# Performance work log

Measured on AMD Instinct MI355X. Metric: run time of the kernel, lower is better.

The kernel has to match this reference:

```python
import jax, jax.numpy as jnp
import numpy as np


def setup_inputs() -> dict:
    key = jax.random.key(0)
    ks = jax.random.split(key, 9)
    n, L, H, H2 = 1024, 256, 512, 256
    return {
        "lstms0": jax.random.normal(ks[0], (n, L), jnp.float32),
        "lstms1": jax.random.normal(ks[1], (n, L), jnp.float32),
        "W_foh": jax.random.normal(ks[2], (2 * L, H), jnp.float32) * 0.05,
        "W_fom": jax.random.normal(ks[3], (2 * L, H), jnp.float32) * 0.05,
        "catBias": jax.random.normal(ks[4], (1, 2 * H), jnp.float32) * 0.05,
        "hid2Layer": jax.random.normal(ks[5], (2 * H, H2), jnp.float32) * 0.05,
        "hid2Bias": jax.random.normal(ks[6], (1, H2), jnp.float32) * 0.05,
        "outLayer": jax.random.normal(ks[7], (H2, 1), jnp.float32) * 0.05,
        "outBias": jax.random.normal(ks[8], (1, 1), jnp.float32) * 0.05,
    }


def reference(lstms0, lstms1, W_foh, W_fom, catBias, hid2Layer, hid2Bias, outLayer, outBias):
    act = jnp.tanh
    H = W_foh.shape[1]
    # per-token concatenated BiLSTM state: [n, 2L]
    x = jnp.concatenate([lstms0, lstms1], axis=-1)
    headfov = x @ W_foh  # [n, H]
    modfov = x @ W_fom   # [n, H]
    # activation(concat(head_i, mod_j) + catBias) is elementwise, so it splits:
    ah = act(headfov + catBias[0, :H])  # [n, H]
    am = act(modfov + catBias[0, H:])   # [n, H]
    # concat(ah_i, am_j) @ hid2Layer == ah_i @ W_top + am_j @ W_bot
    A = ah @ hid2Layer[:H]  # [n, H2]
    B = am @ hid2Layer[H:]  # [n, H2]
    # pairwise hidden: [n_head, n_mod, H2]
    Z = act(A[:, None, :] + B[None, :, :] + hid2Bias[0])
    scores = jnp.einsum("ijh,h->ij", Z, outLayer[:, 0]) + outBias[0, 0]
    return scores  # [n, n], scores[i, j] = score(head=i, mod=j)
```

## Files before the change

### kernel.cpp

```cpp
#include <hip/hip_runtime.h>
#include <hip/hip_bf16.h>

typedef short s16x4 __attribute__((ext_vector_type(4)));
typedef short s16x8 __attribute__((ext_vector_type(8)));
typedef float f32x4 __attribute__((ext_vector_type(4)));

#define LOG2E_2 2.8853900817779268f

__device__ __forceinline__ float fexp2(float x){ return __builtin_amdgcn_exp2f(x); }
__device__ __forceinline__ float frcp (float x){ return __builtin_amdgcn_rcpf(x); }
__device__ __forceinline__ float ftanh(float v){
    return 1.0f - 2.0f * frcp(1.0f + fexp2(LOG2E_2 * v));
}
__device__ __forceinline__ unsigned short f2bf(float v){
    __hip_bfloat16 h = __float2bfloat16(v);
    return __builtin_bit_cast(unsigned short, h);
}
__device__ __forceinline__ float bf2f(unsigned short u){
    return __bfloat162float(__builtin_bit_cast(__hip_bfloat16, u));
}
__device__ __forceinline__ f32x4 mfma32(s16x8 a, s16x8 b, f32x4 c){
    return __builtin_amdgcn_mfma_f32_16x16x32_bf16(a, b, c, 0, 0, 0);
}

__global__ __launch_bounds__(256) void prep_x(
    const float* __restrict__ l0, const float* __restrict__ l1,
    unsigned short* __restrict__ xhi, unsigned short* __restrict__ xlo)
{
    int idx = (blockIdx.x * 256 + threadIdx.x) * 4;
    int r = idx >> 9, c = idx & 511;
    float4 v = (c < 256) ? *(const float4*)(l0 + r*256 + c)
                         : *(const float4*)(l1 + r*256 + (c - 256));
    ushort4 h, l;
    h.x = f2bf(v.x); l.x = f2bf(v.x - bf2f(h.x));
    h.y = f2bf(v.y); l.y = f2bf(v.y - bf2f(h.y));
    h.z = f2bf(v.z); l.z = f2bf(v.z - bf2f(h.z));
    h.w = f2bf(v.w); l.w = f2bf(v.w - bf2f(h.w));
    *(ushort4*)(xhi + idx) = h;
    *(ushort4*)(xlo + idx) = l;
}

__global__ __launch_bounds__(256) void prep_wt(
    const float* __restrict__ srcA, const float* __restrict__ srcB,
    int splitN, int lda, int K,
    unsigned short* __restrict__ dhi, unsigned short* __restrict__ dlo)
{
    __shared__ float F[32][33];
    const int t = threadIdx.x;
    const int k0 = blockIdx.x * 32, n0 = blockIdx.y * 32;
    {
        int kk = t >> 3, n4 = (t & 7) * 4;
        int n = n0 + n4;
        const float* s = (n < splitN) ? (srcA + (k0+kk)*lda + n)
                                      : (srcB + (k0+kk)*lda + (n - splitN));
        float4 v = *(const float4*)s;
        F[kk][n4+0] = v.x; F[kk][n4+1] = v.y; F[kk][n4+2] = v.z; F[kk][n4+3] = v.w;
    }
    __syncthreads();
    {
        int nn = t >> 3, k4 = (t & 7) * 4;
        ushort4 h, l;
        float v0 = F[k4+0][nn]; h.x = f2bf(v0); l.x = f2bf(v0 - bf2f(h.x));
        float v1 = F[k4+1][nn]; h.y = f2bf(v1); l.y = f2bf(v1 - bf2f(h.y));
        float v2 = F[k4+2][nn]; h.z = f2bf(v2); l.z = f2bf(v2 - bf2f(h.z));
        float v3 = F[k4+3][nn]; h.w = f2bf(v3); l.w = f2bf(v3 - bf2f(h.w));
        *(ushort4*)(dhi + (n0+nn)*K + k0 + k4) = h;
        *(ushort4*)(dlo + (n0+nn)*K + k0 + k4) = l;
    }
}

__global__ __launch_bounds__(256) void k1_mfma(
    const unsigned short* __restrict__ xhi, const unsigned short* __restrict__ xlo,
    const unsigned short* __restrict__ whi, const unsigned short* __restrict__ wlo,
    const float* __restrict__ cb,
    unsigned short* __restrict__ hvhi, unsigned short* __restrict__ hvlo)
{
    __shared__ unsigned short Ah[64][40], Al[64][40], Bh[32][40], Bl[32][40];
    const int t = threadIdx.x;
    const int r0 = blockIdx.y * 64, c0 = blockIdx.x * 32;
    const int w = t >> 6, lane = t & 63;
    const int m = lane & 15, quad = lane >> 4;

    const int arow = t >> 2, aseg = t & 3;
    const int brow = (t & 127) >> 2, bseg = t & 3;
    const bool doB = (t < 128);

    f32x4 acc0 = {0,0,0,0}, acc1 = {0,0,0,0};

    const unsigned short* pAh = xhi + (r0+arow)*512 + aseg*8;
    const unsigned short* pAl = xlo + (r0+arow)*512 + aseg*8;
    const unsigned short* pBh = whi + (c0+brow)*512 + bseg*8;
    const unsigned short* pBl = wlo + (c0+brow)*512 + bseg*8;

    uint4 pah = *(const uint4*)pAh;
    uint4 pal = *(const uint4*)pAl;
    uint4 pbh = {}, pbl = {};
    if (doB) { pbh = *(const uint4*)pBh; pbl = *(const uint4*)pBl; }

    for (int c = 0; c < 16; ++c) {
        __syncthreads();
        *(uint4*)&Ah[arow][aseg*8] = pah;
        *(uint4*)&Al[arow][aseg*8] = pal;
        if (doB) {
            *(uint4*)&Bh[brow][bseg*8] = pbh;
            *(uint4*)&Bl[brow][bseg*8] = pbl;
        }
        __syncthreads();
        if (c + 1 < 16) {
            int k0 = (c+1) * 32;
            pah = *(const uint4*)(pAh + k0);
            pal = *(const uint4*)(pAl + k0);
            if (doB) {
                pbh = *(const uint4*)(pBh + k0);
                pbl = *(const uint4*)(pBl + k0);
            }
        }
        {
            const int ko = quad*8;
            s16x8 ah  = *(const s16x8*)&Ah[w*16 + m][ko];
            s16x8 al  = *(const s16x8*)&Al[w*16 + m][ko];
            s16x8 b0h = *(const s16x8*)&Bh[m][ko];
            s16x8 b0l = *(const s16x8*)&Bl[m][ko];
            s16x8 b1h = *(const s16x8*)&Bh[16 + m][ko];
            s16x8 b1l = *(const s16x8*)&Bl[16 + m][ko];
            acc0 = mfma32(ah, b0h, acc0);
            acc0 = mfma32(ah, b0l, acc0);
            acc0 = mfma32(al, b0h, acc0);
            acc1 = mfma32(ah, b1h, acc1);
            acc1 = mfma32(ah, b1l, acc1);
            acc1 = mfma32(al, b1h, acc1);
        }
    }

    #pragma unroll
    for (int nt = 0; nt < 2; ++nt) {
        f32x4 a = nt ? acc1 : acc0;
        const int col = c0 + nt*16 + m;
        const float bias = cb[col];
        #pragma unroll
        for (int reg = 0; reg < 4; ++reg) {
            const int row = r0 + w*16 + quad*4 + reg;
            float v = ftanh(a[reg] + bias);
            unsigned short h = f2bf(v);
            unsigned short l = f2bf(v - bf2f(h));
            hvhi[row*1024 + col] = h;
            hvlo[row*1024 + col] = l;
        }
    }
}

__global__ __launch_bounds__(256) void k2_mfma(
    const unsigned short* __restrict__ hvhi, const unsigned short* __restrict__ hvlo,
    const unsigned short* __restrict__ w2hi, const unsigned short* __restrict__ w2lo,
    const float* __restrict__ h2b, float* __restrict__ P)
{
    __shared__ unsigned short Ah[64][40], Al[64][40], Bh[32][40], Bl[32][40];
    const int t = threadIdx.x;
    const int r0 = blockIdx.y * 64, c0 = blockIdx.x * 32;
    const int half = (c0 >= 256) ? 1 : 0;
    const int ho = half * 512;
    const int nw = c0 & 255;
    const int w = t >> 6, lane = t & 63;
    const int m = lane & 15, quad = lane >> 4;

    const int arow = t >> 2, aseg = t & 3;
    const int brow = (t & 127) >> 2, bseg = t & 3;
    const bool doB = (t < 128);

    f32x4 acc0 = {0,0,0,0}, acc1 = {0,0,0,0};

    const unsigned short* pAh = hvhi + (r0+arow)*1024 + ho + aseg*8;
    const unsigned short* pAl = hvlo + (r0+arow)*1024 + ho + aseg*8;
    const unsigned short* pBh = w2hi + (nw+brow)*1024 + ho + bseg*8;
    const unsigned short* pBl = w2lo + (nw+brow)*1024 + ho + bseg*8;

    uint4 pah = *(const uint4*)pAh;
    uint4 pal = *(const uint4*)pAl;
    uint4 pbh = {}, pbl = {};
    if (doB) { pbh = *(const uint4*)pBh; pbl = *(const uint4*)pBl; }

    for (int c = 0; c < 16; ++c) {
        __syncthreads();
        *(uint4*)&Ah[arow][aseg*8] = pah;
        *(uint4*)&Al[arow][aseg*8] = pal;
        if (doB) {
            *(uint4*)&Bh[brow][bseg*8] = pbh;
            *(uint4*)&Bl[brow][bseg*8] = pbl;
        }
        __syncthreads();
        if (c + 1 < 16) {
            int k0 = (c+1) * 32;
            pah = *(const uint4*)(pAh + k0);
            pal = *(const uint4*)(pAl + k0);
            if (doB) {
                pbh = *(const uint4*)(pBh + k0);
                pbl = *(const uint4*)(pBl + k0);
            }
        }
        {
            const int ko = quad*8;
            s16x8 ah  = *(const s16x8*)&Ah[w*16 + m][ko];
            s16x8 al  = *(const s16x8*)&Al[w*16 + m][ko];
            s16x8 b0h = *(const s16x8*)&Bh[m][ko];
            s16x8 b0l = *(const s16x8*)&Bl[m][ko];
            s16x8 b1h = *(const s16x8*)&Bh[16 + m][ko];
            s16x8 b1l = *(const s16x8*)&Bl[16 + m][ko];
            acc0 = mfma32(ah, b0h, acc0);
            acc0 = mfma32(ah, b0l, acc0);
            acc0 = mfma32(al, b0h, acc0);
            acc1 = mfma32(ah, b1h, acc1);
            acc1 = mfma32(ah, b1l, acc1);
            acc1 = mfma32(al, b1h, acc1);
        }
    }

    #pragma unroll
    for (int nt = 0; nt < 2; ++nt) {
        f32x4 a = nt ? acc1 : acc0;
        const int col = c0 + nt*16 + m;
        const float bias = half ? 0.0f : h2b[col];
        #pragma unroll
        for (int reg = 0; reg < 4; ++reg) {
            const int row = r0 + w*16 + quad*4 + reg;
            P[row*512 + col] = fexp2((a[reg] + bias) * LOG2E_2);
        }
    }
}

__global__ __launch_bounds__(256) void k3_pairwise(
    const float* __restrict__ P, const float* __restrict__ w,
    const float* __restrict__ ob, float* __restrict__ out)
{
    __shared__ float As[32][68];
    __shared__ float Bs[64][34];
    __shared__ float wls[256];
    const int tid = threadIdx.x;
    const int tx = tid & 15;
    const int ty = tid >> 4;
    const int i0 = blockIdx.y * 32, j0 = blockIdx.x * 32;

    wls[tid] = w[tid];

    int rr0 = tid >> 4,        c40 = (tid & 15) * 4;
    int rr1 = (tid + 256) >> 4, c41 = (tid & 15) * 4;

    float acc[2][2] = {};

    float4 pa0 = *(const float4*)&P[(i0+rr0)*512 + 0 + c40];
    float4 pa1 = *(const float4*)&P[(i0+rr1)*512 + 0 + c41];
    float4 pb0 = *(const float4*)&P[(j0+rr0)*512 + 256 + 0 + c40];
    float4 pb1 = *(const float4*)&P[(j0+rr1)*512 + 256 + 0 + c41];

    for (int c = 0; c < 4; ++c) {
        __syncthreads();
        *(float4*)&As[rr0][c40] = pa0;
        *(float4*)&As[rr1][c41] = pa1;
        Bs[c40+0][rr0] = pb0.x; Bs[c40+1][rr0] = pb0.y;
        Bs[c40+2][rr0] = pb0.z; Bs[c40+3][rr0] = pb0.w;
        Bs[c41+0][rr1] = pb1.x; Bs[c41+1][rr1] = pb1.y;
        Bs[c41+2][rr1] = pb1.z; Bs[c41+3][rr1] = pb1.w;
        __syncthreads();
        if (c + 1 < 4) {
            int h0 = (c+1) * 64;
            pa0 = *(const float4*)&P[(i0+rr0)*512 + h0 + c40];
            pa1 = *(const float4*)&P[(i0+rr1)*512 + h0 + c41];
            pb0 = *(const float4*)&P[(j0+rr0)*512 + 256 + h0 + c40];
            pb1 = *(const float4*)&P[(j0+rr1)*512 + 256 + h0 + c41];
        }

        for (int hh = 0; hh < 64; hh += 4) {
            float4 wv = *(const float4*)&wls[c*64 + hh];
            float4 a0 = *(const float4*)&As[ty*2+0][hh];
            float4 a1 = *(const float4*)&As[ty*2+1][hh];
            float2 b0 = *(const float2*)&Bs[hh+0][tx*2];
            float2 b1 = *(const float2*)&Bs[hh+1][tx*2];
            float2 b2 = *(const float2*)&Bs[hh+2][tx*2];
            float2 b3 = *(const float2*)&Bs[hh+3][tx*2];
            float aa[2][4] = {{a0.x,a0.y,a0.z,a0.w},{a1.x,a1.y,a1.z,a1.w}};
            float bb[4][2] = {{b0.x,b0.y},{b1.x,b1.y},{b2.x,b2.y},{b3.x,b3.y}};
            float ww[4] = {wv.x, wv.y, wv.z, wv.w};
            #pragma unroll
            for (int h = 0; h < 4; ++h)
                #pragma unroll
                for (int r = 0; r < 2; ++r)
                    #pragma unroll
                    for (int q = 0; q < 2; ++q) {
                        float u = fmaf(aa[r][h], bb[h][q], 1.0f);
                        acc[r][q] = fmaf(ww[h], frcp(u), acc[r][q]);
                    }
        }
    }

    float sumw = 0.0f;
    #pragma unroll
    for (int h = 0; h < 256; h += 4) {
        float4 wv = *(const float4*)&wls[h];
        sumw += (wv.x + wv.y) + (wv.z + wv.w);
    }
    const float base = ob[0] + sumw;
    const int row = i0 + ty*2;
    const int col = j0 + tx*2;
    #pragma unroll
    for (int r = 0; r < 2; ++r) {
        float2 o;
        o.x = base - 2.0f*acc[r][0];
        o.y = base - 2.0f*acc[r][1];
        *(float2*)&out[(row+r)*1024 + col] = o;
    }
}

extern "C" void kernel_launch(void* const* d_in, const int* in_sizes, int n_in,
                              void* d_out, int out_size, void* d_ws, size_t ws_size,
                              hipStream_t stream) {
    const float* l0   = (const float*)d_in[0];
    const float* l1   = (const float*)d_in[1];
    const float* Wfoh = (const float*)d_in[2];
    const float* Wfom = (const float*)d_in[3];
    const float* cb   = (const float*)d_in[4];
    const float* W2   = (const float*)d_in[5];
    const float* h2b  = (const float*)d_in[6];
    const float* w    = (const float*)d_in[7];
    const float* ob   = (const float*)d_in[8];
    float* out = (float*)d_out;

    unsigned short* hv_hi  = (unsigned short*)d_ws;
    unsigned short* hv_lo  = hv_hi + 1024*1024;
    float*          P      = (float*)(hv_lo + 1024*1024);
    unsigned short* xs_hi  = (unsigned short*)(P + 1024*512);
    unsigned short* xs_lo  = xs_hi + 1024*512;
    unsigned short* w1t_hi = xs_lo + 1024*512;
    unsigned short* w1t_lo = w1t_hi + 1024*512;
    unsigned short* w2t_hi = w1t_lo + 1024*512;
    unsigned short* w2t_lo = w2t_hi + 256*1024;

    prep_x<<<512, 256, 0, stream>>>(l0, l1, xs_hi, xs_lo);
    prep_wt<<<dim3(16,32), 256, 0, stream>>>(Wfoh, Wfom, 512, 512, 512, w1t_hi, w1t_lo);
    prep_wt<<<dim3(32,8),  256, 0, stream>>>(W2, W2, 1<<30, 256, 1024, w2t_hi, w2t_lo);
    k1_mfma<<<dim3(32,16), 256, 0, stream>>>(xs_hi, xs_lo, w1t_hi, w1t_lo, cb, hv_hi, hv_lo);
    k2_mfma<<<dim3(16,16), 256, 0, stream>>>(hv_hi, hv_lo, w2t_hi, w2t_lo, h2b, P);
    k3_pairwise<<<dim3(32,32), 256, 0, stream>>>(P, w, ob, out);
}
```

Measured before the change: 131.0 us.

## Fuse bf16 split conversion into GEMM loads and retile pairwise kernel

Removes the three prep kernels by converting fp32 inputs and weights to hi/lo bf16 pairs while loading tiles inside the two MFMA GEMMs. The hidden activations are packed as interleaved hi/lo in one 32-bit array. The pairwise kernel now uses 64-row tiles, 4x2 outputs per thread and double-buffered shared memory with one barrier per step. This cuts launch count and intermediate traffic, but the GEMMs now do redundant conversion work and transposed scalar LDS stores, and the pairwise kernel uses more registers and LDS.

```diff
diff --git a/kernel.cpp b/kernel.cpp
--- a/kernel.cpp
+++ b/kernel.cpp
@@ -1,7 +1,6 @@
 #include <hip/hip_runtime.h>
 #include <hip/hip_bf16.h>
 
-typedef short s16x4 __attribute__((ext_vector_type(4)));
 typedef short s16x8 __attribute__((ext_vector_type(8)));
 typedef float f32x4 __attribute__((ext_vector_type(4)));
 
@@ -22,58 +21,17 @@
 __device__ __forceinline__ f32x4 mfma32(s16x8 a, s16x8 b, f32x4 c){
     return __builtin_amdgcn_mfma_f32_16x16x32_bf16(a, b, c, 0, 0, 0);
 }
-
-__global__ __launch_bounds__(256) void prep_x(
-    const float* __restrict__ l0, const float* __restrict__ l1,
-    unsigned short* __restrict__ xhi, unsigned short* __restrict__ xlo)
-{
-    int idx = (blockIdx.x * 256 + threadIdx.x) * 4;
-    int r = idx >> 9, c = idx & 511;
-    float4 v = (c < 256) ? *(const float4*)(l0 + r*256 + c)
-                         : *(const float4*)(l1 + r*256 + (c - 256));
-    ushort4 h, l;
+__device__ __forceinline__ void cvt4(float4 v, ushort4& h, ushort4& l){
     h.x = f2bf(v.x); l.x = f2bf(v.x - bf2f(h.x));
     h.y = f2bf(v.y); l.y = f2bf(v.y - bf2f(h.y));
     h.z = f2bf(v.z); l.z = f2bf(v.z - bf2f(h.z));
     h.w = f2bf(v.w); l.w = f2bf(v.w - bf2f(h.w));
-    *(ushort4*)(xhi + idx) = h;
-    *(ushort4*)(xlo + idx) = l;
-}
-
-__global__ __launch_bounds__(256) void prep_wt(
-    const float* __restrict__ srcA, const float* __restrict__ srcB,
-    int splitN, int lda, int K,
-    unsigned short* __restrict__ dhi, unsigned short* __restrict__ dlo)
-{
-    __shared__ float F[32][33];
-    const int t = threadIdx.x;
-    const int k0 = blockIdx.x * 32, n0 = blockIdx.y * 32;
-    {
-        int kk = t >> 3, n4 = (t & 7) * 4;
-        int n = n0 + n4;
-        const float* s = (n < splitN) ? (srcA + (k0+kk)*lda + n)
-                                      : (srcB + (k0+kk)*lda + (n - splitN));
-        float4 v = *(const float4*)s;
-        F[kk][n4+0] = v.x; F[kk][n4+1] = v.y; F[kk][n4+2] = v.z; F[kk][n4+3] = v.w;
-    }
-    __syncthreads();
-    {
-        int nn = t >> 3, k4 = (t & 7) * 4;
-        ushort4 h, l;
-        float v0 = F[k4+0][nn]; h.x = f2bf(v0); l.x = f2bf(v0 - bf2f(h.x));
-        float v1 = F[k4+1][nn]; h.y = f2bf(v1); l.y = f2bf(v1 - bf2f(h.y));
-        float v2 = F[k4+2][nn]; h.z = f2bf(v2); l.z = f2bf(v2 - bf2f(h.z));
-        float v3 = F[k4+3][nn]; h.w = f2bf(v3); l.w = f2bf(v3 - bf2f(h.w));
-        *(ushort4*)(dhi + (n0+nn)*K + k0 + k4) = h;
-        *(ushort4*)(dlo + (n0+nn)*K + k0 + k4) = l;
-    }
 }
 
 __global__ __launch_bounds__(256) void k1_mfma(
-    const unsigned short* __restrict__ xhi, const unsigned short* __restrict__ xlo,
-    const unsigned short* __restrict__ whi, const unsigned short* __restrict__ wlo,
-    const float* __restrict__ cb,
-    unsigned short* __restrict__ hvhi, unsigned short* __restrict__ hvlo)
+    const float* __restrict__ l0, const float* __restrict__ l1,
+    const float* __restrict__ Wfoh, const float* __restrict__ Wfom,
+    const float* __restrict__ cb, unsigned int* __restrict__ hv)
 {
     __shared__ unsigned short Ah[64][40], Al[64][40], Bh[32][40], Bl[32][40];
     const int t = threadIdx.x;
@@ -81,39 +39,44 @@
     const int w = t >> 6, lane = t & 63;
     const int m = lane & 15, quad = lane >> 4;
 
-    const int arow = t >> 2, aseg = t & 3;
-    const int brow = (t & 127) >> 2, bseg = t & 3;
-    const bool doB = (t < 128);
+    const int ar = t >> 3, ak4 = (t & 7) * 4;
+    const int bk = t >> 3, bn4 = (t & 7) * 4;
 
     f32x4 acc0 = {0,0,0,0}, acc1 = {0,0,0,0};
 
-    const unsigned short* pAh = xhi + (r0+arow)*512 + aseg*8;
-    const unsigned short* pAl = xlo + (r0+arow)*512 + aseg*8;
-    const unsigned short* pBh = whi + (c0+brow)*512 + bseg*8;
-    const unsigned short* pBl = wlo + (c0+brow)*512 + bseg*8;
-
-    uint4 pah = *(const uint4*)pAh;
-    uint4 pal = *(const uint4*)pAl;
-    uint4 pbh = {}, pbl = {};
-    if (doB) { pbh = *(const uint4*)pBh; pbl = *(const uint4*)pBl; }
+    ushort4 a0h, a0l, a1h, a1l, bh4, bl4;
+    {
+        int gk = 0 + ak4;
+        float4 va0 = (gk < 256) ? *(const float4*)(l0 + (r0+ar)*256 + gk)
+                                : *(const float4*)(l1 + (r0+ar)*256 + gk - 256);
+        float4 va1 = (gk < 256) ? *(const float4*)(l0 + (r0+ar+32)*256 + gk)
+                                : *(const float4*)(l1 + (r0+ar+32)*256 + gk - 256);
+        int n = c0 + bn4;
+        float4 vb = (n < 512) ? *(const float4*)(Wfoh + (0+bk)*512 + n)
+                              : *(const float4*)(Wfom + (0+bk)*512 + n - 512);
+        cvt4(va0, a0h, a0l); cvt4(va1, a1h, a1l); cvt4(vb, bh4, bl4);
+    }
 
     for (int c = 0; c < 16; ++c) {
         __syncthreads();
-        *(uint4*)&Ah[arow][aseg*8] = pah;
-        *(uint4*)&Al[arow][aseg*8] = pal;
-        if (doB) {
-            *(uint4*)&Bh[brow][bseg*8] = pbh;
-            *(uint4*)&Bl[brow][bseg*8] = pbl;
-        }
+        *(ushort4*)&Ah[ar][ak4]    = a0h;  *(ushort4*)&Al[ar][ak4]    = a0l;
+        *(ushort4*)&Ah[ar+32][ak4] = a1h;  *(ushort4*)&Al[ar+32][ak4] = a1l;
+        Bh[bn4+0][bk] = bh4.x; Bh[bn4+1][bk] = bh4.y;
+        Bh[bn4+2][bk] = bh4.z; Bh[bn4+3][bk] = bh4.w;
+        Bl[bn4+0][bk] = bl4.x; Bl[bn4+1][bk] = bl4.y;
+        Bl[bn4+2][bk] = bl4.z; Bl[bn4+3][bk] = bl4.w;
         __syncthreads();
         if (c + 1 < 16) {
             int k0 = (c+1) * 32;
-            pah = *(const uint4*)(pAh + k0);
-            pal = *(const uint4*)(pAl + k0);
-            if (doB) {
-                pbh = *(const uint4*)(pBh + k0);
-                pbl = *(const uint4*)(pBl + k0);
-            }
+            int gk = k0 + ak4;
+            float4 va0 = (gk < 256) ? *(const float4*)(l0 + (r0+ar)*256 + gk)
+                                    : *(const float4*)(l1 + (r0+ar)*256 + gk - 256);
+            float4 va1 = (gk < 256) ? *(const float4*)(l0 + (r0+ar+32)*256 + gk)
+                                    : *(const float4*)(l1 + (r0+ar+32)*256 + gk - 256);
+            int n = c0 + bn4;
+            float4 vb = (n < 512) ? *(const float4*)(Wfoh + (k0+bk)*512 + n)
+                                  : *(const float4*)(Wfom + (k0+bk)*512 + n - 512);
+            cvt4(va0, a0h, a0l); cvt4(va1, a1h, a1l); cvt4(vb, bh4, bl4);
         }
         {
             const int ko = quad*8;
@@ -143,15 +106,13 @@
             float v = ftanh(a[reg] + bias);
             unsigned short h = f2bf(v);
             unsigned short l = f2bf(v - bf2f(h));
-            hvhi[row*1024 + col] = h;
-            hvlo[row*1024 + col] = l;
+            hv[row*1024 + col] = (unsigned int)h | ((unsigned int)l << 16);
         }
     }
 }
 
 __global__ __launch_bounds__(256) void k2_mfma(
-    const unsigned short* __restrict__ hvhi, const unsigned short* __restrict__ hvlo,
-    const unsigned short* __restrict__ w2hi, const unsigned short* __restrict__ w2lo,
+    const unsigned int* __restrict__ hv, const float* __restrict__ W2,
     const float* __restrict__ h2b, float* __restrict__ P)
 {
     __shared__ unsigned short Ah[64][40], Al[64][40], Bh[32][40], Bl[32][40];
@@ -163,39 +124,42 @@
     const int w = t >> 6, lane = t & 63;
     const int m = lane & 15, quad = lane >> 4;
 
-    const int arow = t >> 2, aseg = t & 3;
-    const int brow = (t & 127) >> 2, bseg = t & 3;
-    const bool doB = (t < 128);
+    const int ar = t >> 3, ak4 = (t & 7) * 4;
+    const int bk = t >> 3, bn4 = (t & 7) * 4;
 
     f32x4 acc0 = {0,0,0,0}, acc1 = {0,0,0,0};
 
-    const unsigned short* pAh = hvhi + (r0+arow)*1024 + ho + aseg*8;
-    const unsigned short* pAl = hvlo + (r0+arow)*1024 + ho + aseg*8;
-    const unsigned short* pBh = w2hi + (nw+brow)*1024 + ho + bseg*8;
-    const unsigned short* pBl = w2lo + (nw+brow)*1024 + ho + bseg*8;
-
-    uint4 pah = *(const uint4*)pAh;
-    uint4 pal = *(const uint4*)pAl;
-    uint4 pbh = {}, pbl = {};
-    if (doB) { pbh = *(const uint4*)pBh; pbl = *(const uint4*)pBl; }
+    ushort4 a0h, a0l, a1h, a1l, bh4, bl4;
+    {
+        uint4 p0 = *(const uint4*)(hv + (r0+ar)*1024 + ho + ak4);
+        uint4 p1 = *(const uint4*)(hv + (r0+ar+32)*1024 + ho + ak4);
+        a0h = make_ushort4(p0.x & 0xffff, p0.y & 0xffff, p0.z & 0xffff, p0.w & 0xffff);
+        a0l = make_ushort4(p0.x >> 16,    p0.y >> 16,    p0.z >> 16,    p0.w >> 16);
+        a1h = make_ushort4(p1.x & 0xffff, p1.y & 0xffff, p1.z & 0xffff, p1.w & 0xffff);
+        a1l = make_ushort4(p1.x >> 16,    p1.y >> 16,    p1.z >> 16,    p1.w >> 16);
+        float4 vb = *(const float4*)(W2 + (ho+bk)*256 + nw + bn4);
+        cvt4(vb, bh4, bl4);
+    }
 
     for (int c = 0; c < 16; ++c) {
         __syncthreads();
-        *(uint4*)&Ah[arow][aseg*8] = pah;
-        *(uint4*)&Al[arow][aseg*8] = pal;
-        if (doB) {
-            *(uint4*)&Bh[brow][bseg*8] = pbh;
-            *(uint4*)&Bl[brow][bseg*8] = pbl;
-        }
+        *(ushort4*)&Ah[ar][ak4]    = a0h;  *(ushort4*)&Al[ar][ak4]    = a0l;
+        *(ushort4*)&Ah[ar+32][ak4] = a1h;  *(ushort4*)&Al[ar+32][ak4] = a1l;
+        Bh[bn4+0][bk] = bh4.x; Bh[bn4+1][bk] = bh4.y;
+        Bh[bn4+2][bk] = bh4.z; Bh[bn4+3][bk] = bh4.w;
+        Bl[bn4+0][bk] = bl4.x; Bl[bn4+1][bk] = bl4.y;
+        Bl[bn4+2][bk] = bl4.z; Bl[bn4+3][bk] = bl4.w;
         __syncthreads();
         if (c + 1 < 16) {
             int k0 = (c+1) * 32;
-            pah = *(const uint4*)(pAh + k0);
-            pal = *(const uint4*)(pAl + k0);
-            if (doB) {
-                pbh = *(const uint4*)(pBh + k0);
-                pbl = *(const uint4*)(pBl + k0);
-            }
+            uint4 p0 = *(const uint4*)(hv + (r0+ar)*1024 + ho + k0 + ak4);
+            uint4 p1 = *(const uint4*)(hv + (r0+ar+32)*1024 + ho + k0 + ak4);
+            a0h = make_ushort4(p0.x & 0xffff, p0.y & 0xffff, p0.z & 0xffff, p0.w & 0xffff);
+            a0l = make_ushort4(p0.x >> 16,    p0.y >> 16,    p0.z >> 16,    p0.w >> 16);
+            a1h = make_ushort4(p1.x & 0xffff, p1.y & 0xffff, p1.z & 0xffff, p1.w & 0xffff);
+            a1l = make_ushort4(p1.x >> 16,    p1.y >> 16,    p1.z >> 16,    p1.w >> 16);
+            float4 vb = *(const float4*)(W2 + (ho+k0+bk)*256 + nw + bn4);
+            cvt4(vb, bh4, bl4);
         }
         {
             const int ko = quad*8;
@@ -231,64 +195,94 @@
     const float* __restrict__ P, const float* __restrict__ w,
     const float* __restrict__ ob, float* __restrict__ out)
 {
-    __shared__ float As[32][68];
-    __shared__ float Bs[64][34];
+    __shared__ float As[2][64][68];
+    __shared__ float Bt[2][64][34];
     __shared__ float wls[256];
     const int tid = threadIdx.x;
     const int tx = tid & 15;
     const int ty = tid >> 4;
-    const int i0 = blockIdx.y * 32, j0 = blockIdx.x * 32;
-
+    const int i0 = blockIdx.y * 64, j0 = blockIdx.x * 32;
+
+    const int arr = tid >> 4, ac4 = (tid & 15) * 4;
+    const int jrr = tid >> 4, jc4 = (tid & 15) * 4;
+
+    float4 pa[4];
+    float4 pb[2];
+
+    #pragma unroll
+    for (int it = 0; it < 4; ++it)
+        pa[it] = *(const float4*)&P[(i0 + arr + it*16)*512 + 0 + ac4];
+    #pragma unroll
+    for (int it = 0; it < 2; ++it)
+        pb[it] = *(const float4*)&P[(j0 + ((jrr + it*16) & 31))*512 + 256 + 0 + jc4 + ((jrr + it*16) >> 5)*64*0];
     wls[tid] = w[tid];
 
-    int rr0 = tid >> 4,        c40 = (tid & 15) * 4;
-    int rr1 = (tid + 256) >> 4, c41 = (tid & 15) * 4;
-
-    float acc[2][2] = {};
-
-    float4 pa0 = *(const float4*)&P[(i0+rr0)*512 + 0 + c40];
-    float4 pa1 = *(const float4*)&P[(i0+rr1)*512 + 0 + c41];
-    float4 pb0 = *(const float4*)&P[(j0+rr0)*512 + 256 + 0 + c40];
-    float4 pb1 = *(const float4*)&P[(j0+rr1)*512 + 256 + 0 + c41];
+    #pragma unroll
+    for (int it = 0; it < 4; ++it)
+        *(float4*)&As[0][arr + it*16][ac4] = pa[it];
+    #pragma unroll
+    for (int it = 0; it < 2; ++it) {
+        int jr = jrr + it*16;
+        Bt[0][jc4+0][jr] = pb[it].x;
+        Bt[0][jc4+1][jr] = pb[it].y;
+        Bt[0][jc4+2][jr] = pb[it].z;
+        Bt[0][jc4+3][jr] = pb[it].w;
+    }
+    __syncthreads();
+
+    float acc[4][2] = {};
 
     for (int c = 0; c < 4; ++c) {
-        __syncthreads();
-        *(float4*)&As[rr0][c40] = pa0;
-        *(float4*)&As[rr1][c41] = pa1;
-        Bs[c40+0][rr0] = pb0.x; Bs[c40+1][rr0] = pb0.y;
-        Bs[c40+2][rr0] = pb0.z; Bs[c40+3][rr0] = pb0.w;
-        Bs[c41+0][rr1] = pb1.x; Bs[c41+1][rr1] = pb1.y;
-        Bs[c41+2][rr1] = pb1.z; Bs[c41+3][rr1] = pb1.w;
-        __syncthreads();
         if (c + 1 < 4) {
             int h0 = (c+1) * 64;
-            pa0 = *(const float4*)&P[(i0+rr0)*512 + h0 + c40];
-            pa1 = *(const float4*)&P[(i0+rr1)*512 + h0 + c41];
-            pb0 = *(const float4*)&P[(j0+rr0)*512 + 256 + h0 + c40];
-            pb1 = *(const float4*)&P[(j0+rr1)*512 + 256 + h0 + c41];
-        }
-
+            #pragma unroll
+            for (int it = 0; it < 4; ++it)
+                pa[it] = *(const float4*)&P[(i0 + arr + it*16)*512 + h0 + ac4];
+            #pragma unroll
+            for (int it = 0; it < 2; ++it)
+                pb[it] = *(const float4*)&P[(j0 + jrr + it*16)*512 + 256 + h0 + jc4];
+        }
+        const int buf = c & 1;
+        #pragma unroll
         for (int hh = 0; hh < 64; hh += 4) {
             float4 wv = *(const float4*)&wls[c*64 + hh];
-            float4 a0 = *(const float4*)&As[ty*2+0][hh];
-            float4 a1 = *(const float4*)&As[ty*2+1][hh];
-            float2 b0 = *(const float2*)&Bs[hh+0][tx*2];
-            float2 b1 = *(const float2*)&Bs[hh+1][tx*2];
-            float2 b2 = *(const float2*)&Bs[hh+2][tx*2];
-            float2 b3 = *(const float2*)&Bs[hh+3][tx*2];
-            float aa[2][4] = {{a0.x,a0.y,a0.z,a0.w},{a1.x,a1.y,a1.z,a1.w}};
+            float4 a0 = *(const float4*)&As[buf][ty*4+0][hh];
+            float4 a1 = *(const float4*)&As[buf][ty*4+1][hh];
+            float4 a2 = *(const float4*)&As[buf][ty*4+2][hh];
+            float4 a3 = *(const float4*)&As[buf][ty*4+3][hh];
+            float2 b0 = *(const float2*)&Bt[buf][hh+0][tx*2];
+            float2 b1 = *(const float2*)&Bt[buf][hh+1][tx*2];
+            float2 b2 = *(const float2*)&Bt[buf][hh+2][tx*2];
+            float2 b3 = *(const float2*)&Bt[buf][hh+3][tx*2];
+            float aa[4][4] = {{a0.x,a0.y,a0.z,a0.w},{a1.x,a1.y,a1.z,a1.w},
+                              {a2.x,a2.y,a2.z,a2.w},{a3.x,a3.y,a3.z,a3.w}};
             float bb[4][2] = {{b0.x,b0.y},{b1.x,b1.y},{b2.x,b2.y},{b3.x,b3.y}};
             float ww[4] = {wv.x, wv.y, wv.z, wv.w};
             #pragma unroll
             for (int h = 0; h < 4; ++h)
                 #pragma unroll
-                for (int r = 0; r < 2; ++r)
+                for (int r = 0; r < 4; ++r)
                     #pragma unroll
                     for (int q = 0; q < 2; ++q) {
                         float u = fmaf(aa[r][h], bb[h][q], 1.0f);
                         acc[r][q] = fmaf(ww[h], frcp(u), acc[r][q]);
                     }
         }
+        if (c + 1 < 4) {
+            const int nbuf = (c+1) & 1;
+            #pragma unroll
+            for (int it = 0; it < 4; ++it)
+                *(float4*)&As[nbuf][arr + it*16][ac4] = pa[it];
+            #pragma unroll
+            for (int it = 0; it < 2; ++it) {
+                int jr = jrr + it*16;
+                Bt[nbuf][jc4+0][jr] = pb[it].x;
+                Bt[nbuf][jc4+1][jr] = pb[it].y;
+                Bt[nbuf][jc4+2][jr] = pb[it].z;
+                Bt[nbuf][jc4+3][jr] = pb[it].w;
+            }
+            __syncthreads();
+        }
     }
 
     float sumw = 0.0f;
@@ -298,14 +292,14 @@
         sumw += (wv.x + wv.y) + (wv.z + wv.w);
     }
     const float base = ob[0] + sumw;
-    const int row = i0 + ty*2;
+    const int row0 = i0 + ty*4;
     const int col = j0 + tx*2;
     #pragma unroll
-    for (int r = 0; r < 2; ++r) {
+    for (int r = 0; r < 4; ++r) {
         float2 o;
         o.x = base - 2.0f*acc[r][0];
         o.y = base - 2.0f*acc[r][1];
-        *(float2*)&out[(row+r)*1024 + col] = o;
+        *(float2*)&out[(row0+r)*1024 + col] = o;
     }
 }
 
@@ -323,20 +317,10 @@
     const float* ob   = (const float*)d_in[8];
     float* out = (float*)d_out;
 
-    unsigned short* hv_hi  = (unsigned short*)d_ws;
-    unsigned short* hv_lo  = hv_hi + 1024*1024;
-    float*          P      = (float*)(hv_lo + 1024*1024);
-    unsigned short* xs_hi  = (unsigned short*)(P + 1024*512);
-    unsigned short* xs_lo  = xs_hi + 1024*512;
-    unsigned short* w1t_hi = xs_lo + 1024*512;
-    unsigned short* w1t_lo = w1t_hi + 1024*512;
-    unsigned short* w2t_hi = w1t_lo + 1024*512;
-    unsigned short* w2t_lo = w2t_hi + 256*1024;
-
-    prep_x<<<512, 256, 0, stream>>>(l0, l1, xs_hi, xs_lo);
-    prep_wt<<<dim3(16,32), 256, 0, stream>>>(Wfoh, Wfom, 512, 512, 512, w1t_hi, w1t_lo);
-    prep_wt<<<dim3(32,8),  256, 0, stream>>>(W2, W2, 1<<30, 256, 1024, w2t_hi, w2t_lo);
-    k1_mfma<<<dim3(32,16), 256, 0, stream>>>(xs_hi, xs_lo, w1t_hi, w1t_lo, cb, hv_hi, hv_lo);
-    k2_mfma<<<dim3(16,16), 256, 0, stream>>>(hv_hi, hv_lo, w2t_hi, w2t_lo, h2b, P);
-    k3_pairwise<<<dim3(32,32), 256, 0, stream>>>(P, w, ob, out);
-}
+    unsigned int* hv = (unsigned int*)d_ws;
+    float*        P  = (float*)(hv + 1024*1024);
+
+    k1_mfma<<<dim3(32,16), 256, 0, stream>>>(l0, l1, Wfoh, Wfom, cb, hv);
+    k2_mfma<<<dim3(16,16), 256, 0, stream>>>(hv, W2, h2b, P);
+    k3_pairwise<<<dim3(32,16), 256, 0, stream>>>(P, w, ob, out);
+}
```

Result: slower. 154.9 us (+18.2%).
